# Optimization experiments

Hardware: AMD Instinct MI355X
Metric: run time of the kernel (lower is better)

The kernel has to match this reference:

```python
import jax, jax.numpy as jnp
import numpy as np

LRELU_SLOPE = 0.2
T_OUT = 10  # opt.train_out_seq


def _lrelu(x):
    return jnp.where(x >= 0, x, LRELU_SLOPE * x)


def _conv(x, w, b, stride, pad):
    y = jax.lax.conv_general_dilated(
        x, w, (stride, stride), [(pad, pad), (pad, pad)],
        dimension_numbers=('NCHW', 'OIHW', 'NCHW'))
    return y + b[None, :, None, None]


def _deconv(x, w, b):
    # ConvTranspose2d(k=4, stride=2, pad=1) expressed as lhs-dilated conv;
    # w is stored in equivalent-conv OIHW form [out, in, 4, 4].
    y = jax.lax.conv_general_dilated(
        x, w, (1, 1), [(2, 2), (2, 2)], lhs_dilation=(2, 2),
        dimension_numbers=('NCHW', 'OIHW', 'NCHW'))
    return y + b[None, :, None, None]


def setup_inputs() -> dict:
    key = jax.random.key(0)
    ks = jax.random.split(key, 10)

    def w(k, shape):
        fan_in = float(np.prod(shape[1:]))
        return (jax.random.normal(k, shape, jnp.float32) / np.sqrt(fan_in))

    B, T_in, C, H = 32, 10, 1, 128
    CE, CG, CH = 16, 64, 64  # chan, conv_encoder_out_ch, convgru_out_ch
    DC = 32  # decoder mid channels (chan*2)
    return {
        'x': jax.random.normal(ks[0], (B, T_in, C, H, H), jnp.float32),
        'enc_w1': w(ks[1], (CE, C, 3, 3)), 'enc_b1': jnp.zeros((CE,), jnp.float32),
        'enc_w2': w(ks[2], (CG, CE, 3, 3)), 'enc_b2': jnp.zeros((CG,), jnp.float32),
        'enc_gru_wzr': w(ks[3], (2 * CH, CG + CH, 5, 5)), 'enc_gru_bzr': jnp.zeros((2 * CH,), jnp.float32),
        'enc_gru_wc': w(ks[4], (CH, CG + CH, 5, 5)), 'enc_gru_bc': jnp.zeros((CH,), jnp.float32),
        'dec_gru_wzr': w(ks[5], (2 * CH, 2 * CH, 5, 5)), 'dec_gru_bzr': jnp.zeros((2 * CH,), jnp.float32),
        'dec_gru_wc': w(ks[6], (CH, 2 * CH, 5, 5)), 'dec_gru_bc': jnp.zeros((CH,), jnp.float32),
        'dec_w1': w(ks[7], (DC, CH, 4, 4)), 'dec_b1': jnp.zeros((DC,), jnp.float32),
        'dec_w2': w(ks[8], (C, DC, 4, 4)), 'dec_b2': jnp.zeros((C,), jnp.float32),
    }


def _forward(x, enc_w1, enc_b1, enc_w2, enc_b2,
             enc_gru_wzr, enc_gru_bzr, enc_gru_wc, enc_gru_bc,
             dec_gru_wzr, dec_gru_bzr, dec_gru_wc, dec_gru_bc,
             dec_w1, dec_b1, dec_w2, dec_b2):
    B, T, C, H, W = x.shape
    CH = enc_gru_wc.shape[0]

    # ---- Encoder convs over all frames ----
    e = _lrelu(_conv(x.reshape(B * T, C, H, W), enc_w1, enc_b1, 2, 1))
    e = _lrelu(_conv(e, enc_w2, enc_b2, 2, 1))  # [B*T, CG, H/4, W/4]
    _, CG, eh, ew = e.shape
    e = e.reshape(B, T, CG, eh, ew).transpose(1, 0, 2, 3, 4)  # [T, B, CG, eh, ew]

    # ---- Encoder ConvGRU over input frames ----
    h0 = jnp.zeros((B, CH, eh, ew), x.dtype)

    def enc_step(h, xt):
        comb = jnp.concatenate([xt, h], axis=1)
        zr = jax.nn.sigmoid(_conv(comb, enc_gru_wzr, enc_gru_bzr, 1, 2))
        r, z = jnp.split(zr, 2, axis=1)
        cand = jnp.tanh(_conv(jnp.concatenate([xt, r * h], axis=1), enc_gru_wc, enc_gru_bc, 1, 2))
        hn = (1.0 - z) * h + z * cand
        return hn, hn

    h_last, _ = jax.lax.scan(enc_step, h0, e)

    # ---- Decoder ConvGRU unrolled with zero inputs (cell(None, h_prev)) ----
    # zero input contributes nothing; use hidden-slice of the gate weights.
    wzr_h, wc_h = dec_gru_wzr[:, CH:], dec_gru_wc[:, CH:]

    def dec_step(h, _):
        zr = jax.nn.sigmoid(_conv(h, wzr_h, dec_gru_bzr, 1, 2))
        r, z = jnp.split(zr, 2, axis=1)
        cand = jnp.tanh(_conv(r * h, wc_h, dec_gru_bc, 1, 2))
        hn = (1.0 - z) * h + z * cand
        return hn, hn

    _, hs = jax.lax.scan(dec_step, h_last, None, length=T_OUT)  # [T_out, B, CH, eh, ew]

    # ---- Decoder transposed convs ----
    y = _lrelu(_deconv(hs.reshape(T_OUT * B, CH, eh, ew), dec_w1, dec_b1))
    y = _deconv(y, dec_w2, dec_b2)  # [T_out*B, C, H, W]
    _, c, oh, ow = y.shape
    return y.reshape(T_OUT, B, c, oh, ow).transpose(1, 0, 2, 3, 4)  # [B, T_out, C, H, W]


def reference(x, enc_w1, enc_b1, enc_w2, enc_b2,
              enc_gru_wzr, enc_gru_bzr, enc_gru_wc, enc_gru_bc,
              dec_gru_wzr, dec_gru_bzr, dec_gru_wc, dec_gru_bc,
              dec_w1, dec_b1, dec_w2, dec_b2):
    return _forward(x, enc_w1, enc_b1, enc_w2, enc_b2,
                    enc_gru_wzr, enc_gru_bzr, enc_gru_wc, enc_gru_bc,
                    dec_gru_wzr, dec_gru_bzr, dec_gru_wc, dec_gru_bc,
                    dec_w1, dec_b1, dec_w2, dec_b2)
```

## Files before the change

### kernel.cpp

```cpp
#include <hip/hip_runtime.h>
#include <math.h>

#define LRELU(v) ((v) >= 0.f ? (v) : 0.2f*(v))

__device__ __forceinline__ float sigmoidf_(float x){ return 1.f/(1.f + expf(-x)); }

typedef __attribute__((ext_vector_type(8))) short bf16x8;
typedef __attribute__((ext_vector_type(4))) float f32x4;
typedef __attribute__((ext_vector_type(8))) unsigned short u16x8;
typedef __attribute__((ext_vector_type(4))) unsigned short u16x4;

__device__ __forceinline__ unsigned short bf16_rne(float x){
    union { float f; unsigned u; } v; v.f = x;
    unsigned r = v.u + 0x7fffu + ((v.u >> 16) & 1u);
    return (unsigned short)(r >> 16);
}
__device__ __forceinline__ float bf16_tof(unsigned short h){
    union { float f; unsigned u; } v; v.u = ((unsigned)h) << 16; return v.f;
}
__device__ __forceinline__ void bsplit(float x, unsigned short& hi, unsigned short& lo){
    hi = bf16_rne(x);
    lo = bf16_rne(x - bf16_tof(hi));
}

__global__ __launch_bounds__(256) void k_conv1(const float* __restrict__ x,
    const float* __restrict__ W, const float* __restrict__ Bb, float* __restrict__ out)
{
    __shared__ float wl[144];
    __shared__ float bl[16];
    int tid = threadIdx.x;
    if (tid < 144) { int oc = tid/9, tap = tid%9; wl[tap*16+oc] = W[oc*9+tap]; }
    if (tid < 16) bl[tid] = Bb[tid];
    __syncthreads();
    int img = blockIdx.y;
    int px = blockIdx.x*256 + tid;
    int oy = px >> 6, ox = px & 63;
    const float* xin = x + (size_t)img*16384;
    float acc[16];
    #pragma unroll
    for (int o=0;o<16;++o) acc[o]=bl[o];
    #pragma unroll
    for (int kh=0; kh<3; ++kh){
        int iy = 2*oy + kh - 1;
        bool vy = (iy>=0 && iy<128);
        #pragma unroll
        for (int kw=0; kw<3; ++kw){
            int ix = 2*ox + kw - 1;
            float v = (vy && ix>=0 && ix<128) ? xin[iy*128+ix] : 0.f;
            int tap = kh*3+kw;
            #pragma unroll
            for (int o=0;o<16;++o) acc[o] += wl[tap*16+o]*v;
        }
    }
    float* op = out + (size_t)img*65536 + px;
    #pragma unroll
    for (int o=0;o<16;++o){ float v = acc[o]; op[o*4096] = LRELU(v); }
}

__global__ __launch_bounds__(256) void k_conv2(const float* __restrict__ in,
    const float* __restrict__ W, const float* __restrict__ Bb,
    unsigned short* __restrict__ e2hi, unsigned short* __restrict__ e2lo)
{
    __shared__ float tile[2*65*68];
    __shared__ float wl[2*9*16];
    int tid = threadIdx.x;
    int img = blockIdx.y;
    int ocBase = blockIdx.x*16;
    int y = tid >> 3, xg = tid & 7, x0 = xg*4;
    float acc[16][4];
    #pragma unroll
    for (int o=0;o<16;++o){ float b = Bb[ocBase+o];
        #pragma unroll
        for (int p=0;p<4;++p) acc[o][p] = b; }
    const float* base = in + (size_t)img*65536;
    for (int icB=0; icB<16; icB+=2){
        for (int e=tid; e<2210; e+=256){
            int c4 = e % 17; int rr = (e/17)%65; int ch = e/(17*65);
            int iy = rr - 1; int ixb = c4*4 - 4;
            float4 v = make_float4(0.f,0.f,0.f,0.f);
            if (iy>=0 && iy<64 && c4>=1)
                v = *(const float4*)(base + (icB+ch)*4096 + iy*64 + ixb);
            *(float4*)(&tile[ch*4420 + rr*68 + c4*4]) = v;
        }
        for (int e=tid; e<288; e+=256){
            int oc = e & 15; int rest = e >> 4; int tap = rest % 9; int ch = rest/9;
            wl[(ch*9+tap)*16 + oc] = W[((ocBase+oc)*16 + icB+ch)*9 + tap];
        }
        __syncthreads();
        #pragma unroll
        for (int ch=0; ch<2; ++ch){
            #pragma unroll
            for (int kh=0; kh<3; ++kh){
                int r = 2*y + kh;
                const float4* row = (const float4*)(&tile[ch*4420 + r*68 + 2*x0]);
                float4 a0=row[0], a1=row[1], a2=row[2];
                float win[12] = {a0.x,a0.y,a0.z,a0.w,a1.x,a1.y,a1.z,a1.w,a2.x,a2.y,a2.z,a2.w};
                #pragma unroll
                for (int kw=0; kw<3; ++kw){
                    const float4* wp = (const float4*)(&wl[(ch*9+kh*3+kw)*16]);
                    float4 w0=wp[0], w1=wp[1], w2=wp[2], w3=wp[3];
                    float wv[16] = {w0.x,w0.y,w0.z,w0.w,w1.x,w1.y,w1.z,w1.w,
                                    w2.x,w2.y,w2.z,w2.w,w3.x,w3.y,w3.z,w3.w};
                    #pragma unroll
                    for (int p=0;p<4;++p){
                        float v = win[2*p + kw + 3];
                        #pragma unroll
                        for (int o=0;o<16;++o) acc[o][p] += wv[o]*v;
                    }
                }
            }
        }
        __syncthreads();
    }
    size_t pxbase = (size_t)img*1024 + y*32 + x0;
    #pragma unroll
    for (int p=0;p<4;++p){
        u16x8 h0v, h1v, l0v, l1v;
        #pragma unroll
        for (int o=0;o<8;++o){
            float v0 = acc[o][p];   v0 = LRELU(v0);
            float v1 = acc[o+8][p]; v1 = LRELU(v1);
            unsigned short hh, ll;
            bsplit(v0,hh,ll); h0v[o]=hh; l0v[o]=ll;
            bsplit(v1,hh,ll); h1v[o]=hh; l1v[o]=ll;
        }
        size_t bo = (pxbase + p)*64 + ocBase;
        *(u16x8*)&e2hi[bo]   = h0v; *(u16x8*)&e2hi[bo+8] = h1v;
        *(u16x8*)&e2lo[bo]   = l0v; *(u16x8*)&e2lo[bo+8] = l1v;
    }
}

__global__ __launch_bounds__(256) void k_prep(const float* __restrict__ W,
    int wIcTot, int wIcOff, int icTot, int total,
    unsigned short* __restrict__ outHi, unsigned short* __restrict__ outLo)
{
    int id = blockIdx.x*256 + threadIdx.x;
    if (id >= total) return;
    int lane = id & 63;
    int grp  = id >> 6;
    int ks = grp % 7;
    int rest = grp / 7;
    int iccTot = icTot >> 3;
    int oc = (rest / iccTot)*16 + (lane & 15);
    int t  = ks*4 + (lane >> 4);
    int icBase = (rest % iccTot)*8;
    u16x8 vh, vl;
    #pragma unroll
    for (int r=0;r<8;++r){
        float v = 0.f;
        if (t < 25) v = W[((size_t)oc*wIcTot + wIcOff + icBase + r)*25 + t];
        unsigned short hh, ll; bsplit(v, hh, ll);
        vh[r]=hh; vl[r]=ll;
    }
    size_t base = ((size_t)grp)*512 + lane*8;
    *(u16x8*)&outHi[base] = vh;
    *(u16x8*)&outLo[base] = vl;
}

__global__ __launch_bounds__(256) void k_prep_d1(const float* __restrict__ W,
    unsigned short* __restrict__ outHi, unsigned short* __restrict__ outLo)
{
    int id = blockIdx.x*256 + threadIdx.x;
    if (id >= 4096) return;
    int lane = id & 63;
    int grp = id >> 6;
    int icc = grp & 7; int par = (grp>>3)&3; int mt = grp>>5;
    int py = par>>1, px = par&1;
    int oc = mt*16 + (lane&15);
    int t = lane>>4; int a = t>>1, bb = t&1;
    int kh = 2*a+py, kw = 2*bb+px;
    u16x8 vh, vl;
    #pragma unroll
    for (int r=0;r<8;++r){
        int ic = icc*8 + r;
        float v = W[(((size_t)oc*64 + ic)*4 + kh)*4 + kw];
        unsigned short hh, ll; bsplit(v, hh, ll);
        vh[r]=hh; vl[r]=ll;
    }
    size_t base = ((size_t)grp)*512 + lane*8;
    *(u16x8*)&outHi[base] = vh;
    *(u16x8*)&outLo[base] = vl;
}

template<int MODE, int ROWS, int NOC>
__global__ __launch_bounds__(256) void k_conv5f(
    const unsigned short* __restrict__ aHi, const unsigned short* __restrict__ aLo,
    unsigned long long strA, int iccA,
    const unsigned short* __restrict__ inbHi, const unsigned short* __restrict__ inbLo,
    unsigned long long strB,
    const unsigned short* __restrict__ wHi, const unsigned short* __restrict__ wLo,
    int iccTot,
    const float* __restrict__ bias,
    const float* __restrict__ h32,
    const float* __restrict__ z32in,
    float* __restrict__ z32out,
    unsigned short* __restrict__ oHi, unsigned short* __restrict__ oLo,
    float* __restrict__ h32out,
    unsigned short* __restrict__ hsHi, unsigned short* __restrict__ hsLo)
{
    constexpr int RW = ROWS/4;
    constexpr int NT = ROWS/2;
    constexpr int SPOS = (ROWS+4)*36;
    constexpr int SPAN = (32/ROWS)*4;
    __shared__ __align__(16) unsigned short ldsHi[2][SPOS*8];
    __shared__ __align__(16) unsigned short ldsLo[2][SPOS*8];
    int tid = threadIdx.x;
    int lane = tid & 63, wave = tid >> 6;
    int bid = blockIdx.x;
    int m = bid & 7;
    int kk = bid >> 3;
    int ocBlk = kk % NOC;
    int g = kk / NOC;
    int idx = m*SPAN + g;
    int batch = idx & 31;
    int r0 = (idx >> 5)*ROWS;

    int sA = tid;
    int lyA = sA/36, lxA = sA - lyA*36;
    int gyA = r0 - 2 + lyA, gxA = lxA - 2;
    bool vA = (gyA>=0 && gyA<32 && gxA>=0 && gxA<32);
    size_t poA = ((size_t)(gyA*32+gxA))*64;
    int sB = tid + 256;
    bool hasB = (sB < SPOS);
    int lyB = sB/36, lxB = sB - lyB*36;
    int gyB = r0 - 2 + lyB, gxB = lxB - 2;
    bool vB = hasB && (gyB>=0 && gyB<32 && gxB>=0 && gxB<32);
    size_t poB = ((size_t)(gyB*32+gxB))*64;

    int offs[7];
    #pragma unroll
    for (int ks=0; ks<7; ++ks){
        int t = ks*4 + (lane>>4);
        int dy = (t<25)? t/5 : 2;
        int dx = (t<25)? t%5 : 2;
        offs[ks] = (dy*36 + dx)*8;
    }
    int eb[NT];
    #pragma unroll
    for (int n=0;n<NT;++n)
        eb[n] = (((wave*RW + (n>>1))*36) + (n&1)*16 + (lane&15))*8;

    f32x4 acc[2][NT];
    #pragma unroll
    for (int mm=0;mm<2;++mm)
      #pragma unroll
      for (int n=0;n<NT;++n) acc[mm][n] = (f32x4){0.f,0.f,0.f,0.f};

    u16x8 rAh=(u16x8)0, rAl=(u16x8)0, rBh=(u16x8)0, rBl=(u16x8)0;

    {
        const unsigned short* sHp; const unsigned short* sLp; int icLoc;
        if (0 < iccA){ sHp = aHi + (size_t)batch*strA; sLp = aLo + (size_t)batch*strA; icLoc = 0; }
        else         { sHp = inbHi + (size_t)batch*strB; sLp = inbLo + (size_t)batch*strB; icLoc = -iccA; }
        if (vA){ rAh = *(const u16x8*)&sHp[poA + icLoc*8]; rAl = *(const u16x8*)&sLp[poA + icLoc*8]; }
        if (vB){ rBh = *(const u16x8*)&sHp[poB + icLoc*8]; rBl = *(const u16x8*)&sLp[poB + icLoc*8]; }
    }
    *(u16x8*)&ldsHi[0][sA*8] = rAh; *(u16x8*)&ldsLo[0][sA*8] = rAl;
    if (hasB){ *(u16x8*)&ldsHi[0][sB*8] = rBh; *(u16x8*)&ldsLo[0][sB*8] = rBl; }

    int cur = 0;
    for (int icc = 0; icc < iccTot; ++icc){
        __syncthreads();
        if (icc+1 < iccTot){
            int icn = icc+1;
            const unsigned short* sHp; const unsigned short* sLp; int icLoc;
            if (icn < iccA){ sHp = aHi + (size_t)batch*strA; sLp = aLo + (size_t)batch*strA; icLoc = icn; }
            else           { sHp = inbHi + (size_t)batch*strB; sLp = inbLo + (size_t)batch*strB; icLoc = icn - iccA; }
            rAh=(u16x8)0; rAl=(u16x8)0; rBh=(u16x8)0; rBl=(u16x8)0;
            if (vA){ rAh = *(const u16x8*)&sHp[poA + icLoc*8]; rAl = *(const u16x8*)&sLp[poA + icLoc*8]; }
            if (vB){ rBh = *(const u16x8*)&sHp[poB + icLoc*8]; rBl = *(const u16x8*)&sLp[poB + icLoc*8]; }
        }
        bf16x8 wv[28];
        #pragma unroll
        for (int ks=0; ks<7; ++ks){
            size_t i0 = (((size_t)(ocBlk*2+0)*iccTot + icc)*7 + ks)*512 + lane*8;
            size_t i1 = (((size_t)(ocBlk*2+1)*iccTot + icc)*7 + ks)*512 + lane*8;
            wv[ks*4+0] = *(const bf16x8*)&wHi[i0];
            wv[ks*4+1] = *(const bf16x8*)&wLo[i0];
            wv[ks*4+2] = *(const bf16x8*)&wHi[i1];
            wv[ks*4+3] = *(const bf16x8*)&wLo[i1];
        }
        const unsigned short* bHp = ldsHi[cur];
        const unsigned short* bLp = ldsLo[cur];
        #pragma unroll
        for (int ks=0; ks<7; ++ks){
            bf16x8 a0h = wv[ks*4+0];
            bf16x8 a0l = wv[ks*4+1];
            bf16x8 a1h = wv[ks*4+2];
            bf16x8 a1l = wv[ks*4+3];
            bf16x8 bh[NT], bl[NT];
            #pragma unroll
            for (int n=0;n<NT;++n){
                int e = eb[n] + offs[ks];
                bh[n] = *(const bf16x8*)&bHp[e];
                bl[n] = *(const bf16x8*)&bLp[e];
            }
            #pragma unroll
            for (int n=0;n<NT;++n){
                acc[0][n] = __builtin_amdgcn_mfma_f32_16x16x32_bf16(a0h, bh[n], acc[0][n], 0,0,0);
                acc[0][n] = __builtin_amdgcn_mfma_f32_16x16x32_bf16(a0h, bl[n], acc[0][n], 0,0,0);
                acc[0][n] = __builtin_amdgcn_mfma_f32_16x16x32_bf16(a0l, bh[n], acc[0][n], 0,0,0);
                acc[1][n] = __builtin_amdgcn_mfma_f32_16x16x32_bf16(a1h, bh[n], acc[1][n], 0,0,0);
                acc[1][n] = __builtin_amdgcn_mfma_f32_16x16x32_bf16(a1h, bl[n], acc[1][n], 0,0,0);
                acc[1][n] = __builtin_amdgcn_mfma_f32_16x16x32_bf16(a1l, bh[n], acc[1][n], 0,0,0);
            }
        }
        if (icc+1 < iccTot){
            int nb = cur ^ 1;
            *(u16x8*)&ldsHi[nb][sA*8] = rAh; *(u16x8*)&ldsLo[nb][sA*8] = rAl;
            if (hasB){ *(u16x8*)&ldsHi[nb][sB*8] = rBh; *(u16x8*)&ldsLo[nb][sB*8] = rBl; }
        }
        cur ^= 1;
    }

    if (MODE == 0){
        bool rside = (ocBlk < 2);
        #pragma unroll
        for (int mm=0;mm<2;++mm){
            int ocBase = ocBlk*32 + mm*16 + (lane>>4)*4;
            f32x4 b4 = *(const f32x4*)&bias[ocBase];
            #pragma unroll
            for (int n=0;n<NT;++n){
                int px = (r0 + wave*RW + (n>>1))*32 + (n&1)*16 + (lane&15);
                if (rside){
                    size_t ii = ((size_t)batch*1024 + px)*64 + ocBase;
                    f32x4 h4 = *(const f32x4*)&h32[ii];
                    u16x4 rH, rL;
                    #pragma unroll
                    for (int j=0;j<4;++j){
                        float r = sigmoidf_(acc[mm][n][j] + b4[j]);
                        unsigned short hh,ll; bsplit(r*h4[j],hh,ll);
                        rH[j]=hh; rL[j]=ll;
                    }
                    *(u16x4*)&oHi[ii] = rH;
                    *(u16x4*)&oLo[ii] = rL;
                } else {
                    size_t ii = ((size_t)batch*1024 + px)*64 + ocBase - 64;
                    f32x4 z;
                    #pragma unroll
                    for (int j=0;j<4;++j) z[j] = sigmoidf_(acc[mm][n][j] + b4[j]);
                    *(f32x4*)&z32out[ii] = z;
                }
            }
        }
    } else {
        #pragma unroll
        for (int mm=0;mm<2;++mm){
            int oc = ocBlk*32 + mm*16 + (lane>>4)*4;
            f32x4 b4 = *(const f32x4*)&bias[oc];
            #pragma unroll
            for (int n=0;n<NT;++n){
                int px = (r0 + wave*RW + (n>>1))*32 + (n&1)*16 + (lane&15);
                size_t ii = ((size_t)batch*1024 + px)*64 + oc;
                f32x4 h4 = *(const f32x4*)&h32[ii];
                f32x4 z4 = *(const f32x4*)&z32in[ii];
                f32x4 hn; u16x4 hh4, hl4;
                #pragma unroll
                for (int j=0;j<4;++j){
                    float c = tanhf(acc[mm][n][j] + b4[j]);
                    hn[j] = (1.f - z4[j])*h4[j] + z4[j]*c;
                    unsigned short hh,ll; bsplit(hn[j],hh,ll);
                    hh4[j]=hh; hl4[j]=ll;
                }
                *(f32x4*)&h32out[ii] = hn;
                *(u16x4*)&oHi[ii] = hh4;
                *(u16x4*)&oLo[ii] = hl4;
                if (hsHi){
                    *(u16x4*)&hsHi[ii] = hh4;
                    *(u16x4*)&hsLo[ii] = hl4;
                }
            }
        }
    }
}

__global__ __launch_bounds__(256) void k_deconv1m(
    const unsigned short* __restrict__ hsHi, const unsigned short* __restrict__ hsLo,
    const unsigned short* __restrict__ wHi, const unsigned short* __restrict__ wLo,
    const float* __restrict__ Bb, float* __restrict__ y1)
{
    __shared__ __align__(16) unsigned short ldsHi[2][340*8];
    __shared__ __align__(16) unsigned short ldsLo[2][340*8];
    int tid = threadIdx.x;
    int lane = tid & 63, wave = tid >> 6;
    int bid = blockIdx.x;
    int m = bid & 7;
    int kk = bid >> 3;
    int par = kk & 3;
    int g = kk >> 2;
    int idx = m*32 + g;
    int tbl = idx & 63;
    int r0 = (idx >> 6)*8;
    int py = par >> 1, px = par & 1;
    const unsigned short* sH = hsHi + (size_t)tbl*65536;
    const unsigned short* sL = hsLo + (size_t)tbl*65536;

    int sA = tid;
    int lyA = sA/34, lxA = sA - lyA*34;
    int gyA = r0 - 1 + lyA, gxA = lxA - 1;
    bool vA = (gyA>=0 && gyA<32 && gxA>=0 && gxA<32);
    size_t poA = ((size_t)(gyA*32+gxA))*64;
    int sB = tid + 256;
    bool hasB = (sB < 340);
    int lyB = sB/34, lxB = sB - lyB*34;
    int gyB = r0 - 1 + lyB, gxB = lxB - 1;
    bool vB = hasB && (gyB>=0 && gyB<32 && gxB>=0 && gxB<32);
    size_t poB = ((size_t)(gyB*32+gxB))*64;

    int offs0 = ((lane>>5)*34 + ((lane>>4)&1))*8;
    int eb[4];
    #pragma unroll
    for (int n=0;n<4;++n)
        eb[n] = (((wave*2 + (n>>1)) + py)*34 + (n&1)*16 + (lane&15) + px)*8;

    f32x4 acc[2][4];
    #pragma unroll
    for (int mm=0;mm<2;++mm)
      #pragma unroll
      for (int n=0;n<4;++n) acc[mm][n] = (f32x4){0.f,0.f,0.f,0.f};

    u16x8 rAh=(u16x8)0, rAl=(u16x8)0, rBh=(u16x8)0, rBl=(u16x8)0;
    if (vA){ rAh = *(const u16x8*)&sH[poA]; rAl = *(const u16x8*)&sL[poA]; }
    if (vB){ rBh = *(const u16x8*)&sH[poB]; rBl = *(const u16x8*)&sL[poB]; }
    *(u16x8*)&ldsHi[0][sA*8] = rAh; *(u16x8*)&ldsLo[0][sA*8] = rAl;
    if (hasB){ *(u16x8*)&ldsHi[0][sB*8] = rBh; *(u16x8*)&ldsLo[0][sB*8] = rBl; }

    int cur = 0;
    for (int icc=0; icc<8; ++icc){
        __syncthreads();
        if (icc+1 < 8){
            size_t co = (size_t)(icc+1)*8;
            rAh=(u16x8)0; rAl=(u16x8)0; rBh=(u16x8)0; rBl=(u16x8)0;
            if (vA){ rAh = *(const u16x8*)&sH[poA + co]; rAl = *(const u16x8*)&sL[poA + co]; }
            if (vB){ rBh = *(const u16x8*)&sH[poB + co]; rBl = *(const u16x8*)&sL[poB + co]; }
        }
        const unsigned short* bHp = ldsHi[cur];
        const unsigned short* bLp = ldsLo[cur];
        size_t i0 = ((size_t)((0*4 + par)*8 + icc))*512 + lane*8;
        size_t i1 = ((size_t)((1*4 + par)*8 + icc))*512 + lane*8;
        bf16x8 a0h = *(const bf16x8*)&wHi[i0];
        bf16x8 a0l = *(const bf16x8*)&wLo[i0];
        bf16x8 a1h = *(const bf16x8*)&wHi[i1];
        bf16x8 a1l = *(const bf16x8*)&wLo[i1];
        bf16x8 bh[4], bl[4];
        #pragma unroll
        for (int n=0;n<4;++n){
            int e = eb[n] + offs0;
            bh[n] = *(const bf16x8*)&bHp[e];
            bl[n] = *(const bf16x8*)&bLp[e];
        }
        #pragma unroll
        for (int n=0;n<4;++n){
            acc[0][n] = __builtin_amdgcn_mfma_f32_16x16x32_bf16(a0h, bh[n], acc[0][n], 0,0,0);
            acc[0][n] = __builtin_amdgcn_mfma_f32_16x16x32_bf16(a0h, bl[n], acc[0][n], 0,0,0);
            acc[0][n] = __builtin_amdgcn_mfma_f32_16x16x32_bf16(a0l, bh[n], acc[0][n], 0,0,0);
            acc[1][n] = __builtin_amdgcn_mfma_f32_16x16x32_bf16(a1h, bh[n], acc[1][n], 0,0,0);
            acc[1][n] = __builtin_amdgcn_mfma_f32_16x16x32_bf16(a1h, bl[n], acc[1][n], 0,0,0);
            acc[1][n] = __builtin_amdgcn_mfma_f32_16x16x32_bf16(a1l, bh[n], acc[1][n], 0,0,0);
        }
        if (icc+1 < 8){
            int nb = cur ^ 1;
            *(u16x8*)&ldsHi[nb][sA*8] = rAh; *(u16x8*)&ldsLo[nb][sA*8] = rAl;
            if (hasB){ *(u16x8*)&ldsHi[nb][sB*8] = rBh; *(u16x8*)&ldsLo[nb][sB*8] = rBl; }
        }
        cur ^= 1;
    }
    #pragma unroll
    for (int mm=0;mm<2;++mm){
        int ocb = mm*16 + (lane>>4)*4;
        #pragma unroll
        for (int n=0;n<4;++n){
            int oyr = r0 + wave*2 + (n>>1);
            int oxc = (n&1)*16 + (lane&15);
            int oy = 2*oyr + py, ox = 2*oxc + px;
            float* dst = y1 + ((size_t)tbl*32 + ocb)*4096 + oy*64 + ox;
            #pragma unroll
            for (int j=0;j<4;++j){
                float v = acc[mm][n][j] + Bb[ocb+j];
                dst[(size_t)j*4096] = LRELU(v);
            }
        }
    }
}

__global__ __launch_bounds__(256) void k_deconv2(const float* __restrict__ in,
    const float* __restrict__ W, const float* __restrict__ Bb, float* __restrict__ out,
    int tbOff)
{
    __shared__ float wl[512];
    int tid = threadIdx.x;
    for (int e=tid; e<512; e+=256) wl[e] = W[e];
    __syncthreads();
    int tbl = blockIdx.y;
    int tb = tbOff + tbl; int t = tb >> 5; int b = tb & 31;
    int idx4 = blockIdx.x*256 + tid;
    int oy = idx4 >> 5; int ox0 = (idx4 & 31)*4;
    int ph = oy & 1;
    const float* base = in + (size_t)tbl*131072;
    float acc0=0.f, acc1=0.f, acc2=0.f, acc3=0.f;
    int ix0 = ox0/2 - 1;
    for (int ic=0; ic<32; ++ic){
        const float* cp = base + ic*4096;
        #pragma unroll
        for (int kk=0; kk<2; ++kk){
            int kh = ph + 2*kk;
            int iy = (oy + kh - 2) >> 1;
            if (iy < 0 || iy > 63) continue;
            const float* rp = cp + (size_t)iy*64;
            float wv0 = (ix0 >= 0)   ? rp[ix0]   : 0.f;
            float wv1 = rp[ix0+1];
            float wv2 = rp[ix0+2];
            float wv3 = (ix0+3 <= 63) ? rp[ix0+3] : 0.f;
            float w0 = wl[ic*16 + kh*4 + 0];
            float w1 = wl[ic*16 + kh*4 + 1];
            float w2 = wl[ic*16 + kh*4 + 2];
            float w3 = wl[ic*16 + kh*4 + 3];
            acc0 += w0*wv0 + w2*wv1;
            acc2 += w0*wv1 + w2*wv2;
            acc1 += w1*wv1 + w3*wv2;
            acc3 += w1*wv2 + w3*wv3;
        }
    }
    float bv = Bb[0];
    float4 res = make_float4(acc0+bv, acc1+bv, acc2+bv, acc3+bv);
    float* op = out + ((size_t)(b*10 + t))*16384 + (size_t)oy*128 + ox0;
    *(float4*)op = res;
}

extern "C" void kernel_launch(void* const* d_in, const int* in_sizes, int n_in,
                              void* d_out, int out_size, void* d_ws, size_t ws_size,
                              hipStream_t stream)
{
    const float* x    = (const float*)d_in[0];
    const float* ew1  = (const float*)d_in[1];
    const float* eb1  = (const float*)d_in[2];
    const float* ew2  = (const float*)d_in[3];
    const float* eb2  = (const float*)d_in[4];
    const float* ewzr = (const float*)d_in[5];
    const float* ebzr = (const float*)d_in[6];
    const float* ewc  = (const float*)d_in[7];
    const float* ebc  = (const float*)d_in[8];
    const float* dwzr = (const float*)d_in[9];
    const float* dbzr = (const float*)d_in[10];
    const float* dwc  = (const float*)d_in[11];
    const float* dbc  = (const float*)d_in[12];
    const float* dw1  = (const float*)d_in[13];
    const float* db1  = (const float*)d_in[14];
    const float* dw2  = (const float*)d_in[15];
    const float* db2  = (const float*)d_in[16];
    float* out = (float*)d_out;
    char* ws = (char*)d_ws;

    unsigned short* e2hi = (unsigned short*)(ws + 0);
    unsigned short* e2lo = (unsigned short*)(ws + 41943040UL);
    float*          h32  = (float*)(ws + 83886080UL);
    unsigned short* hHi  = (unsigned short*)(ws + 92274688UL);
    unsigned short* hLo  = (unsigned short*)(ws + 96468992UL);
    unsigned short* rhHi = (unsigned short*)(ws + 100663296UL);
    unsigned short* rhLo = (unsigned short*)(ws + 104857600UL);
    float*          z32  = (float*)(ws + 109051904UL);
    unsigned short* A0   = (unsigned short*)(ws + 117440512UL);
    unsigned short* AzrH = A0;            unsigned short* AzrL = A0 + 458752;
    unsigned short* AcH  = A0 + 917504;   unsigned short* AcL  = A0 + 1146880;
    unsigned short* DzrH = A0 + 1376256;  unsigned short* DzrL = A0 + 1605632;
    unsigned short* DcH  = A0 + 1835008;  unsigned short* DcL  = A0 + 1949696;
    unsigned short* D1H  = A0 + 2064384;  unsigned short* D1L  = A0 + 2097152;
    float* e1c = (float*)(ws + 83886080UL);
    float* y1c = (float*)(ws + 83886080UL);

    for (int c=0; c<2; ++c){
        int off = c*160;
        k_conv1<<<dim3(16,160),256,0,stream>>>(x + (size_t)off*16384, ew1, eb1, e1c);
        k_conv2<<<dim3(4,160),256,0,stream>>>(e1c, ew2, eb2,
                                              e2hi + (size_t)off*65536,
                                              e2lo + (size_t)off*65536);
    }

    k_prep<<<224,256,0,stream>>>(ewzr, 128, 0, 128, 57344, AzrH, AzrL);
    k_prep<<<112,256,0,stream>>>(ewc,  128, 0, 128, 28672, AcH,  AcL);
    k_prep<<<112,256,0,stream>>>(dwzr, 128, 64, 64, 28672, DzrH, DzrL);
    k_prep<<< 56,256,0,stream>>>(dwc,  128, 64, 64, 14336, DcH,  DcL);
    k_prep_d1<<<16,256,0,stream>>>(dw1, D1H, D1L);

    hipMemsetAsync(h32, 0, 8388608UL, stream);
    hipMemsetAsync(hHi, 0, 4194304UL, stream);
    hipMemsetAsync(hLo, 0, 4194304UL, stream);

    for (int t=0; t<10; ++t){
        k_conv5f<0,8,4><<<512,256,0,stream>>>(
            e2hi + (size_t)t*65536, e2lo + (size_t)t*65536, 655360ULL, 8,
            hHi, hLo, 65536ULL, AzrH, AzrL, 16, ebzr,
            h32, nullptr, z32, rhHi, rhLo, nullptr, nullptr, nullptr);
        k_conv5f<1,4,2><<<512,256,0,stream>>>(
            e2hi + (size_t)t*65536, e2lo + (size_t)t*65536, 655360ULL, 8,
            rhHi, rhLo, 65536ULL, AcH, AcL, 16, ebc,
            h32, z32, nullptr, hHi, hLo, h32, nullptr, nullptr);
    }
    for (int t=0; t<10; ++t){
        k_conv5f<0,8,4><<<512,256,0,stream>>>(
            hHi, hLo, 65536ULL, 8,
            hHi, hLo, 65536ULL, DzrH, DzrL, 8, dbzr,
            h32, nullptr, z32, rhHi, rhLo, nullptr, nullptr, nullptr);
        k_conv5f<1,4,2><<<512,256,0,stream>>>(
            rhHi, rhLo, 65536ULL, 8,
            rhHi, rhLo, 65536ULL, DcH, DcL, 8, dbc,
            h32, z32, nullptr, hHi, hLo, h32,
            e2hi + (size_t)t*2097152, e2lo + (size_t)t*2097152);
    }
    for (int c=0; c<5; ++c){
        int tbOff = c*64;
        k_deconv1m<<<1024,256,0,stream>>>(
            e2hi + (size_t)tbOff*65536, e2lo + (size_t)tbOff*65536,
            D1H, D1L, db1, y1c);
        k_deconv2<<<dim3(16,64),256,0,stream>>>(y1c, dw2, db2, out, tbOff);
    }
}
```

Before: 2.949 ms.

## Move encoder conv2 onto split-bf16 MFMA with channel-last bf16 intermediates

conv1 now writes channel-last hi/lo bf16 pairs instead of planar fp32. The scalar-FMA conv2 is replaced by an MFMA kernel that stages an input halo tile in LDS and multiplies against pre-split weights packed by a new prep kernel, using three bf16 products per term to approximate fp32 accuracy. The encoder is now processed in four chunks of 80 images instead of two of 160. A priority raise (s_setprio) around the MFMA loop in the GRU conv kernel is also added. The main risk is the extra prep launch and the halving of the K dimension to 9 taps padded to 12, which wastes some MFMA work.

```diff
diff --git a/kernel.cpp b/kernel.cpp
--- a/kernel.cpp
+++ b/kernel.cpp
@@ -24,7 +24,8 @@
 }
 
 __global__ __launch_bounds__(256) void k_conv1(const float* __restrict__ x,
-    const float* __restrict__ W, const float* __restrict__ Bb, float* __restrict__ out)
+    const float* __restrict__ W, const float* __restrict__ Bb,
+    unsigned short* __restrict__ e1Hi, unsigned short* __restrict__ e1Lo)
 {
     __shared__ float wl[144];
     __shared__ float bl[16];
@@ -52,81 +53,156 @@
             for (int o=0;o<16;++o) acc[o] += wl[tap*16+o]*v;
         }
     }
-    float* op = out + (size_t)img*65536 + px;
-    #pragma unroll
-    for (int o=0;o<16;++o){ float v = acc[o]; op[o*4096] = LRELU(v); }
-}
-
-__global__ __launch_bounds__(256) void k_conv2(const float* __restrict__ in,
-    const float* __restrict__ W, const float* __restrict__ Bb,
+    size_t bo = ((size_t)img*4096 + px)*16;
+    u16x8 h0, h1, l0, l1;
+    #pragma unroll
+    for (int o=0;o<8;++o){
+        float v0 = LRELU(acc[o]);
+        float v1 = LRELU(acc[o+8]);
+        unsigned short hh, ll;
+        bsplit(v0,hh,ll); h0[o]=hh; l0[o]=ll;
+        bsplit(v1,hh,ll); h1[o]=hh; l1[o]=ll;
+    }
+    *(u16x8*)&e1Hi[bo]   = h0; *(u16x8*)&e1Hi[bo+8] = h1;
+    *(u16x8*)&e1Lo[bo]   = l0; *(u16x8*)&e1Lo[bo+8] = l1;
+}
+
+__global__ __launch_bounds__(256) void k_prep_c2(const float* __restrict__ W,
+    unsigned short* __restrict__ outHi, unsigned short* __restrict__ outLo)
+{
+    int id = blockIdx.x*256 + threadIdx.x;
+    if (id >= 1536) return;
+    int lane = id & 63;
+    int grp = id >> 6;
+    int ks = grp % 3;
+    int icc = (grp/3) & 1;
+    int mt2 = grp / 6;
+    int oc = mt2*16 + (lane & 15);
+    int t = ks*4 + (lane >> 4);
+    u16x8 vh, vl;
+    #pragma unroll
+    for (int r=0;r<8;++r){
+        int ic = icc*8 + r;
+        float v = 0.f;
+        if (t < 9) v = W[(((size_t)oc*16 + ic)*3 + t/3)*3 + (t%3)];
+        unsigned short hh, ll; bsplit(v, hh, ll);
+        vh[r]=hh; vl[r]=ll;
+    }
+    size_t base = ((size_t)grp)*512 + lane*8;
+    *(u16x8*)&outHi[base] = vh;
+    *(u16x8*)&outLo[base] = vl;
+}
+
+__global__ __launch_bounds__(256) void k_conv2m(
+    const unsigned short* __restrict__ e1Hi, const unsigned short* __restrict__ e1Lo,
+    const unsigned short* __restrict__ wHi, const unsigned short* __restrict__ wLo,
+    const float* __restrict__ Bb,
     unsigned short* __restrict__ e2hi, unsigned short* __restrict__ e2lo)
 {
-    __shared__ float tile[2*65*68];
-    __shared__ float wl[2*9*16];
+    __shared__ __align__(16) unsigned short ldsHi[1122*8];
+    __shared__ __align__(16) unsigned short ldsLo[1122*8];
     int tid = threadIdx.x;
-    int img = blockIdx.y;
-    int ocBase = blockIdx.x*16;
-    int y = tid >> 3, xg = tid & 7, x0 = xg*4;
-    float acc[16][4];
-    #pragma unroll
-    for (int o=0;o<16;++o){ float b = Bb[ocBase+o];
-        #pragma unroll
-        for (int p=0;p<4;++p) acc[o][p] = b; }
-    const float* base = in + (size_t)img*65536;
-    for (int icB=0; icB<16; icB+=2){
-        for (int e=tid; e<2210; e+=256){
-            int c4 = e % 17; int rr = (e/17)%65; int ch = e/(17*65);
-            int iy = rr - 1; int ixb = c4*4 - 4;
-            float4 v = make_float4(0.f,0.f,0.f,0.f);
-            if (iy>=0 && iy<64 && c4>=1)
-                v = *(const float4*)(base + (icB+ch)*4096 + iy*64 + ixb);
-            *(float4*)(&tile[ch*4420 + rr*68 + c4*4]) = v;
-        }
-        for (int e=tid; e<288; e+=256){
-            int oc = e & 15; int rest = e >> 4; int tap = rest % 9; int ch = rest/9;
-            wl[(ch*9+tap)*16 + oc] = W[((ocBase+oc)*16 + icB+ch)*9 + tap];
-        }
+    int lane = tid & 63, wave = tid >> 6;
+    int bid = blockIdx.x;
+    int m = bid & 7;
+    int kk = bid >> 3;
+    int ocBlk = kk & 1;
+    int g = kk >> 1;
+    int idx = m*40 + g;
+    int img = idx >> 2;
+    int rt  = idx & 3;
+    int r0 = rt*8;
+
+    const unsigned short* sH = e1Hi + (size_t)img*65536;
+    const unsigned short* sL = e1Lo + (size_t)img*65536;
+
+    int q = lane >> 4;
+    int eb[4];
+    #pragma unroll
+    for (int n=0;n<4;++n){
+        int ro = wave*2 + (n>>1);
+        int oco = (n&1)*16 + (lane&15);
+        eb[n] = (2*ro*66 + 2*oco)*8;
+    }
+    int offs[3];
+    #pragma unroll
+    for (int ks=0; ks<3; ++ks){
+        int t = ks*4 + q;
+        int dy = (t<9)? t/3 : 0;
+        int dx = (t<9)? t%3 : 0;
+        offs[ks] = (dy*66 + dx)*8;
+    }
+
+    f32x4 acc[2][4];
+    #pragma unroll
+    for (int mm=0;mm<2;++mm)
+      #pragma unroll
+      for (int n=0;n<4;++n) acc[mm][n] = (f32x4){0.f,0.f,0.f,0.f};
+
+    for (int icc=0; icc<2; ++icc){
         __syncthreads();
         #pragma unroll
-        for (int ch=0; ch<2; ++ch){
-            #pragma unroll
-            for (int kh=0; kh<3; ++kh){
-                int r = 2*y + kh;
-                const float4* row = (const float4*)(&tile[ch*4420 + r*68 + 2*x0]);
-                float4 a0=row[0], a1=row[1], a2=row[2];
-                float win[12] = {a0.x,a0.y,a0.z,a0.w,a1.x,a1.y,a1.z,a1.w,a2.x,a2.y,a2.z,a2.w};
-                #pragma unroll
-                for (int kw=0; kw<3; ++kw){
-                    const float4* wp = (const float4*)(&wl[(ch*9+kh*3+kw)*16]);
-                    float4 w0=wp[0], w1=wp[1], w2=wp[2], w3=wp[3];
-                    float wv[16] = {w0.x,w0.y,w0.z,w0.w,w1.x,w1.y,w1.z,w1.w,
-                                    w2.x,w2.y,w2.z,w2.w,w3.x,w3.y,w3.z,w3.w};
-                    #pragma unroll
-                    for (int p=0;p<4;++p){
-                        float v = win[2*p + kw + 3];
-                        #pragma unroll
-                        for (int o=0;o<16;++o) acc[o][p] += wv[o]*v;
-                    }
+        for (int k=0;k<5;++k){
+            int s = tid + k*256;
+            if (s < 1122){
+                int ly = s/66, lx = s - ly*66;
+                int gy = 2*r0 - 1 + ly, gx = lx - 1;
+                u16x8 vh=(u16x8)0, vl=(u16x8)0;
+                if (gy>=0 && gy<64 && gx>=0 && gx<64){
+                    size_t off = ((size_t)(gy*64+gx))*16 + icc*8;
+                    vh = *(const u16x8*)&sH[off];
+                    vl = *(const u16x8*)&sL[off];
                 }
+                *(u16x8*)&ldsHi[s*8] = vh;
+                *(u16x8*)&ldsLo[s*8] = vl;
             }
         }
         __syncthreads();
-    }
-    size_t pxbase = (size_t)img*1024 + y*32 + x0;
-    #pragma unroll
-    for (int p=0;p<4;++p){
-        u16x8 h0v, h1v, l0v, l1v;
-        #pragma unroll
-        for (int o=0;o<8;++o){
-            float v0 = acc[o][p];   v0 = LRELU(v0);
-            float v1 = acc[o+8][p]; v1 = LRELU(v1);
-            unsigned short hh, ll;
-            bsplit(v0,hh,ll); h0v[o]=hh; l0v[o]=ll;
-            bsplit(v1,hh,ll); h1v[o]=hh; l1v[o]=ll;
-        }
-        size_t bo = (pxbase + p)*64 + ocBase;
-        *(u16x8*)&e2hi[bo]   = h0v; *(u16x8*)&e2hi[bo+8] = h1v;
-        *(u16x8*)&e2lo[bo]   = l0v; *(u16x8*)&e2lo[bo+8] = l1v;
+        #pragma unroll
+        for (int ks=0; ks<3; ++ks){
+            size_t i0 = (((size_t)(ocBlk*2+0)*2 + icc)*3 + ks)*512 + lane*8;
+            size_t i1 = (((size_t)(ocBlk*2+1)*2 + icc)*3 + ks)*512 + lane*8;
+            bf16x8 a0h = *(const bf16x8*)&wHi[i0];
+            bf16x8 a0l = *(const bf16x8*)&wLo[i0];
+            bf16x8 a1h = *(const bf16x8*)&wHi[i1];
+            bf16x8 a1l = *(const bf16x8*)&wLo[i1];
+            bf16x8 bh[4], bl[4];
+            #pragma unroll
+            for (int n=0;n<4;++n){
+                int e = eb[n] + offs[ks];
+                bh[n] = *(const bf16x8*)&ldsHi[e];
+                bl[n] = *(const bf16x8*)&ldsLo[e];
+            }
+            #pragma unroll
+            for (int n=0;n<4;++n){
+                acc[0][n] = __builtin_amdgcn_mfma_f32_16x16x32_bf16(a0h, bh[n], acc[0][n], 0,0,0);
+                acc[0][n] = __builtin_amdgcn_mfma_f32_16x16x32_bf16(a0h, bl[n], acc[0][n], 0,0,0);
+                acc[0][n] = __builtin_amdgcn_mfma_f32_16x16x32_bf16(a0l, bh[n], acc[0][n], 0,0,0);
+                acc[1][n] = __builtin_amdgcn_mfma_f32_16x16x32_bf16(a1h, bh[n], acc[1][n], 0,0,0);
+                acc[1][n] = __builtin_amdgcn_mfma_f32_16x16x32_bf16(a1h, bl[n], acc[1][n], 0,0,0);
+                acc[1][n] = __builtin_amdgcn_mfma_f32_16x16x32_bf16(a1l, bh[n], acc[1][n], 0,0,0);
+            }
+        }
+    }
+    #pragma unroll
+    for (int mm=0;mm<2;++mm){
+        int oc = ocBlk*32 + mm*16 + (lane>>4)*4;
+        f32x4 b4 = *(const f32x4*)&Bb[oc];
+        #pragma unroll
+        for (int n=0;n<4;++n){
+            int px = (r0 + wave*2 + (n>>1))*32 + (n&1)*16 + (lane&15);
+            size_t ii = ((size_t)img*1024 + px)*64 + oc;
+            u16x4 hh4, hl4;
+            #pragma unroll
+            for (int j=0;j<4;++j){
+                float v = acc[mm][n][j] + b4[j];
+                v = LRELU(v);
+                unsigned short hh,ll; bsplit(v,hh,ll);
+                hh4[j]=hh; hl4[j]=ll;
+            }
+            *(u16x4*)&e2hi[ii] = hh4;
+            *(u16x4*)&e2lo[ii] = hl4;
+        }
     }
 }
 
@@ -282,6 +358,7 @@
         }
         const unsigned short* bHp = ldsHi[cur];
         const unsigned short* bLp = ldsLo[cur];
+        __builtin_amdgcn_s_setprio(1);
         #pragma unroll
         for (int ks=0; ks<7; ++ks){
             bf16x8 a0h = wv[ks*4+0];
@@ -305,6 +382,7 @@
                 acc[1][n] = __builtin_amdgcn_mfma_f32_16x16x32_bf16(a1l, bh[n], acc[1][n], 0,0,0);
             }
         }
+        __builtin_amdgcn_s_setprio(0);
         if (icc+1 < iccTot){
             int nb = cur ^ 1;
             *(u16x8*)&ldsHi[nb][sA*8] = rAh; *(u16x8*)&ldsLo[nb][sA*8] = rAl;
@@ -565,15 +643,20 @@
     unsigned short* DzrH = A0 + 1376256;  unsigned short* DzrL = A0 + 1605632;
     unsigned short* DcH  = A0 + 1835008;  unsigned short* DcL  = A0 + 1949696;
     unsigned short* D1H  = A0 + 2064384;  unsigned short* D1L  = A0 + 2097152;
-    float* e1c = (float*)(ws + 83886080UL);
+    unsigned short* C2H  = A0 + 2129920;  unsigned short* C2L  = A0 + 2142208;
+    unsigned short* e1cH = (unsigned short*)(ws + 83886080UL);
+    unsigned short* e1cL = (unsigned short*)(ws + 94371840UL);
     float* y1c = (float*)(ws + 83886080UL);
 
-    for (int c=0; c<2; ++c){
-        int off = c*160;
-        k_conv1<<<dim3(16,160),256,0,stream>>>(x + (size_t)off*16384, ew1, eb1, e1c);
-        k_conv2<<<dim3(4,160),256,0,stream>>>(e1c, ew2, eb2,
-                                              e2hi + (size_t)off*65536,
-                                              e2lo + (size_t)off*65536);
+    k_prep_c2<<<6,256,0,stream>>>(ew2, C2H, C2L);
+
+    for (int c=0; c<4; ++c){
+        int off = c*80;
+        k_conv1<<<dim3(16,80),256,0,stream>>>(x + (size_t)off*16384, ew1, eb1,
+                                              e1cH, e1cL);
+        k_conv2m<<<640,256,0,stream>>>(e1cH, e1cL, C2H, C2L, eb2,
+                                       e2hi + (size_t)off*65536,
+                                       e2lo + (size_t)off*65536);
     }
 
     k_prep<<<224,256,0,stream>>>(ewzr, 128, 0, 128, 57344, AzrH, AzrL);
```

Measured after the change: 2.797 ms. 5.1% less time.
